# Optimization experiments

Hardware: AMD Instinct MI355X
Metric: run time of the kernel (lower is better)

Reference implementation:

```python
import jax, jax.numpy as jnp
import numpy as np

N_NODES = 50000
N_EDGES = 600000
IN_CH = 128
HID = 128
OUT_CH = 1
N_GRAPHS = 64


def setup_inputs() -> dict:
    key = jax.random.key(0)
    ks = jax.random.split(key, 16)
    inp = {
        "x": jax.random.normal(ks[0], (N_NODES, IN_CH), dtype=jnp.float32),
        "edge_index": jax.random.randint(ks[1], (2, N_EDGES), 0, N_NODES, dtype=jnp.int64),
        "edge_weight": jax.random.uniform(ks[2], (N_EDGES,), dtype=jnp.float32),
        "batch": jnp.sort(jax.random.randint(ks[3], (N_NODES,), 0, N_GRAPHS, dtype=jnp.int64)),
    }
    # SAGEConv params: lin_l (neighbor-aggregate path, has bias) and lin_r (root path)
    dims = [(IN_CH, HID), (HID, HID), (HID, HID), (HID, HID)]
    for i, (din, dout) in enumerate(dims, start=1):
        s = 1.0 / np.sqrt(din)
        inp[f"Wl{i}"] = jax.random.uniform(ks[3 + 2 * i], (din, dout), minval=-s, maxval=s, dtype=jnp.float32)
        inp[f"Wr{i}"] = jax.random.uniform(ks[4 + 2 * i], (din, dout), minval=-s, maxval=s, dtype=jnp.float32)
        inp[f"b{i}"] = jnp.zeros((dout,), dtype=jnp.float32)
    s = 1.0 / np.sqrt(HID)
    inp["Wc"] = jax.random.uniform(ks[14], (HID, OUT_CH), minval=-s, maxval=s, dtype=jnp.float32)
    inp["bc"] = jnp.zeros((OUT_CH,), dtype=jnp.float32)
    return inp


def _sage_conv(x, src, dst, Wl, Wr, b):
    # mean aggregation of source-node features at each destination node
    msg = x[src]  # [E, d] gather
    agg = jax.ops.segment_sum(msg, dst, num_segments=N_NODES)
    cnt = jax.ops.segment_sum(jnp.ones((src.shape[0],), x.dtype), dst, num_segments=N_NODES)
    agg = agg / jnp.maximum(cnt, 1.0)[:, None]
    return agg @ Wl + b + x @ Wr


def reference(x, edge_index, edge_weight, batch,
              Wl1, Wr1, b1, Wl2, Wr2, b2, Wl3, Wr3, b3, Wl4, Wr4, b4, Wc, bc):
    src, dst = edge_index[0], edge_index[1]
    h = jax.nn.relu(_sage_conv(x, src, dst, Wl1, Wr1, b1))
    h = jax.nn.relu(_sage_conv(h, src, dst, Wl2, Wr2, b2))
    h = jax.nn.relu(_sage_conv(h, src, dst, Wl3, Wr3, b3))
    h = jax.nn.relu(_sage_conv(h, src, dst, Wl4, Wr4, b4))
    # global mean pool over graphs
    pooled = jax.ops.segment_sum(h, batch, num_segments=N_GRAPHS)
    gcnt = jax.ops.segment_sum(jnp.ones((N_NODES,), h.dtype), batch, num_segments=N_GRAPHS)
    pooled = pooled / jnp.maximum(gcnt, 1.0)[:, None]  # [G, HID]
    return jax.nn.sigmoid(pooled @ Wc + bc)  # [G, 1]
```

## Files before the change

### kernel.cpp

```cpp
#include <hip/hip_runtime.h>
#include <math.h>

#define NND 50000
#define LNP 50048
#define NED 600000
#define CD  128
#define NG  64
#define NBLK 196
#define GROWS 64

typedef short s8v  __attribute__((ext_vector_type(8)));
typedef float f4v  __attribute__((ext_vector_type(4)));
typedef float f2v  __attribute__((ext_vector_type(2)));
typedef unsigned short u16x4 __attribute__((ext_vector_type(4)));
typedef unsigned short u16x8 __attribute__((ext_vector_type(8)));

static __device__ __forceinline__ unsigned short f2bf(float f) {
  union { float f; unsigned u; } v; v.f = f;
  unsigned r = v.u + 0x7fffu + ((v.u >> 16) & 1u);
  return (unsigned short)(r >> 16);
}
static __device__ __forceinline__ unsigned short f2bf_t(float f) {
  union { float f; unsigned u; } v; v.f = f;
  return (unsigned short)(v.u >> 16);
}
static __device__ __forceinline__ unsigned f2fp8x4(float a, float b, float c, float d) {
  int r = __builtin_amdgcn_cvt_pk_fp8_f32(a, b, 0, false);
  r = __builtin_amdgcn_cvt_pk_fp8_f32(c, d, r, true);
  return (unsigned)r;
}
static __device__ __forceinline__ s8v fp8x8_to_bf16(uint2 v) {
  f2v c0 = __builtin_amdgcn_cvt_pk_f32_fp8(v.x, false);
  f2v c1 = __builtin_amdgcn_cvt_pk_f32_fp8(v.x, true);
  f2v c2 = __builtin_amdgcn_cvt_pk_f32_fp8(v.y, false);
  f2v c3 = __builtin_amdgcn_cvt_pk_f32_fp8(v.y, true);
  union { u16x8 u; s8v s; } o;
  o.u[0] = f2bf_t(c0.x); o.u[1] = f2bf_t(c0.y);
  o.u[2] = f2bf_t(c1.x); o.u[3] = f2bf_t(c1.y);
  o.u[4] = f2bf_t(c2.x); o.u[5] = f2bf_t(c2.y);
  o.u[6] = f2bf_t(c3.x); o.u[7] = f2bf_t(c3.y);
  return o.s;
}
static __device__ __forceinline__ void g2lds8(const unsigned char* g, unsigned char* l) {
  __builtin_amdgcn_global_load_lds(
      (const __attribute__((address_space(1))) unsigned*)g,
      (__attribute__((address_space(3))) unsigned*)l, 16, 0, 0);
}

__global__ __launch_bounds__(256) void bsum_k(const int* __restrict__ cnt,
                                              int* __restrict__ bsum) {
  __shared__ int s[256];
  int i = blockIdx.x * 256 + threadIdx.x;
  s[threadIdx.x] = (i < NND) ? cnt[i] : 0;
  __syncthreads();
  for (int off = 128; off > 0; off >>= 1) {
    if (threadIdx.x < off) s[threadIdx.x] += s[threadIdx.x + off];
    __syncthreads();
  }
  if (threadIdx.x == 0) bsum[blockIdx.x] = s[0];
}

__global__ __launch_bounds__(256) void bscan_k(const int* __restrict__ bsum,
                                               int* __restrict__ boff,
                                               int* __restrict__ offs,
                                               const int* __restrict__ batch,
                                               int* __restrict__ gb) {
  __shared__ int s[256];
  int t = threadIdx.x;
  if (t <= NG) {
    int lo = 0, hi = NND;
    while (lo < hi) {
      int mid = (lo + hi) >> 1;
      if (batch[mid] < t) lo = mid + 1; else hi = mid;
    }
    gb[t] = lo;
  }
  s[t] = (t < NBLK) ? bsum[t] : 0;
  __syncthreads();
  for (int off = 1; off < 256; off <<= 1) {
    int v = (t >= off) ? s[t - off] : 0;
    __syncthreads();
    s[t] += v;
    __syncthreads();
  }
  if (t < NBLK) boff[t] = (t == 0) ? 0 : s[t - 1];
  if (t == NBLK - 1) offs[NND] = s[t];
}

__global__ __launch_bounds__(256) void escan_k(const int* __restrict__ cnt,
                                               const int* __restrict__ boff,
                                               int* __restrict__ offs,
                                               int* __restrict__ cur) {
  __shared__ int s[256];
  int i = blockIdx.x * 256 + threadIdx.x;
  int t = threadIdx.x;
  int v = (i < NND) ? cnt[i] : 0;
  s[t] = v;
  __syncthreads();
  for (int off = 1; off < 256; off <<= 1) {
    int u = (t >= off) ? s[t - off] : 0;
    __syncthreads();
    s[t] += u;
    __syncthreads();
  }
  if (i < NND) {
    int excl = s[t] - v + boff[blockIdx.x];
    offs[i] = excl;
    cur[i]  = excl;
  }
}

__global__ void fill_k(const int* __restrict__ src, const int* __restrict__ dst,
                       int* __restrict__ cur, int* __restrict__ csr) {
  int e = blockIdx.x * blockDim.x + threadIdx.x;
  if (e >= NED) return;
  int d = dst[e];
  int pos = atomicAdd(&cur[d], 1);
  csr[pos] = src[e];
}

struct WPtrs { const float* w[8]; unsigned short* wt[8]; };
__global__ void prep_k(const float* __restrict__ x, unsigned* __restrict__ x8,
                       WPtrs p, const int* __restrict__ dst, int* __restrict__ cnt) {
  int t = blockIdx.x * blockDim.x + threadIdx.x;
  if (t < NND * 32) {
    float4 v = reinterpret_cast<const float4*>(x)[t];
    x8[t] = f2fp8x4(v.x, v.y, v.z, v.w);
  } else {
    int u = t - NND * 32;
    if (u < 8 * CD * CD) {
      int m = u >> 14, r = u & (CD * CD - 1);
      int n = r >> 7, k = r & 127;
      p.wt[m][r] = f2bf(p.w[m][k * CD + n]);
    } else {
      int e = u - 8 * CD * CD;
      if (e < NED) atomicAdd(&cnt[dst[e]], 1);
    }
  }
}

__global__ __launch_bounds__(256, 4) void sage_k(
    const unsigned* __restrict__ xq,
    const int* __restrict__ csr, const int* __restrict__ offs,
    const unsigned short* __restrict__ WlT, const unsigned short* __restrict__ WrT,
    const float* __restrict__ bias, unsigned char* __restrict__ h8,
    const int* __restrict__ batch, float* __restrict__ pooled) {
  __shared__ unsigned short abuf[GROWS * CD];
  __shared__ unsigned char  x8buf[GROWS * CD];
  __shared__ int sB[GROWS];

  const int tid  = threadIdx.x;
  const int wave = tid >> 6;
  const int lane = tid & 63;
  const int quad = lane >> 4;
  const int l16  = lane & 15;
  const size_t rbase = (size_t)blockIdx.x * GROWS;

  {
    const unsigned char* xg = (const unsigned char*)xq;
#pragma unroll
    for (int j = 0; j < 2; ++j) {
      const int s = j * 256 + tid;
      g2lds8(xg + (rbase + (s >> 3)) * CD + (s & 7) * 16, &x8buf[(size_t)s * 16]);
    }
  }

  if (pooled && tid < GROWS) {
    size_t row = rbase + tid;
    sB[tid] = (row < NND) ? batch[row] : -1;
  }

  s8v bL[2][4], bR[2][4];
#pragma unroll
  for (int nt = 0; nt < 2; ++nt) {
    const int n = wave * 32 + nt * 16 + l16;
#pragma unroll
    for (int kk = 0; kk < 4; ++kk) {
      size_t woff = (size_t)n * CD + kk * 32 + quad * 8;
      bL[nt][kk] = *reinterpret_cast<const s8v*>(WlT + woff);
      bR[nt][kk] = *reinterpret_cast<const s8v*>(WrT + woff);
    }
  }
  const float bv0 = bias[wave * 32 + l16];
  const float bv1 = bias[wave * 32 + 16 + l16];

  {
    const int team = tid >> 3;
    const int tl   = tid & 7;
    const unsigned* base = xq + tl * 4;
    for (int i = 0; i < 2; ++i) {
      const int rl = team * 2 + i;
      const size_t row = rbase + rl;
      u16x8 o0 = {}, o1 = {};
      if (row < NND) {
        const int e0 = offs[row], e1 = offs[row + 1];
        f2v a[8] = {};
        int e = e0;
        for (; e + 4 <= e1; e += 4) {
          int s[4];
#pragma unroll
          for (int j = 0; j < 4; ++j) s[j] = csr[e + j];
          uint4 v[4];
#pragma unroll
          for (int j = 0; j < 4; ++j)
            v[j] = *reinterpret_cast<const uint4*>(base + (size_t)s[j] * 32);
#pragma unroll
          for (int j = 0; j < 4; ++j) {
            a[0] += __builtin_amdgcn_cvt_pk_f32_fp8(v[j].x, false);
            a[1] += __builtin_amdgcn_cvt_pk_f32_fp8(v[j].x, true);
            a[2] += __builtin_amdgcn_cvt_pk_f32_fp8(v[j].y, false);
            a[3] += __builtin_amdgcn_cvt_pk_f32_fp8(v[j].y, true);
            a[4] += __builtin_amdgcn_cvt_pk_f32_fp8(v[j].z, false);
            a[5] += __builtin_amdgcn_cvt_pk_f32_fp8(v[j].z, true);
            a[6] += __builtin_amdgcn_cvt_pk_f32_fp8(v[j].w, false);
            a[7] += __builtin_amdgcn_cvt_pk_f32_fp8(v[j].w, true);
          }
        }
        for (; e < e1; ++e) {
          uint4 v = *reinterpret_cast<const uint4*>(base + (size_t)csr[e] * 32);
          a[0] += __builtin_amdgcn_cvt_pk_f32_fp8(v.x, false);
          a[1] += __builtin_amdgcn_cvt_pk_f32_fp8(v.x, true);
          a[2] += __builtin_amdgcn_cvt_pk_f32_fp8(v.y, false);
          a[3] += __builtin_amdgcn_cvt_pk_f32_fp8(v.y, true);
          a[4] += __builtin_amdgcn_cvt_pk_f32_fp8(v.z, false);
          a[5] += __builtin_amdgcn_cvt_pk_f32_fp8(v.z, true);
          a[6] += __builtin_amdgcn_cvt_pk_f32_fp8(v.w, false);
          a[7] += __builtin_amdgcn_cvt_pk_f32_fp8(v.w, true);
        }
        const float invd = 1.0f / fmaxf((float)(e1 - e0), 1.0f);
#pragma unroll
        for (int c = 0; c < 4; ++c) {
          o0[2 * c]     = f2bf(a[c].x * invd);
          o0[2 * c + 1] = f2bf(a[c].y * invd);
          o1[2 * c]     = f2bf(a[4 + c].x * invd);
          o1[2 * c + 1] = f2bf(a[4 + c].y * invd);
        }
      }
      *reinterpret_cast<u16x8*>(abuf + rl * CD + tl * 16)     = o0;
      *reinterpret_cast<u16x8*>(abuf + rl * CD + tl * 16 + 8) = o1;
    }
  }

  __syncthreads();

  const bool fast = pooled && (rbase + GROWS <= NND) && (sB[0] == sB[GROWS - 1]);
  const int c0 = wave * 32 + l16;
  float p0 = 0.f, p1 = 0.f;

#pragma unroll
  for (int rt = 0; rt < GROWS / 16; ++rt) {
    const unsigned short* arow = abuf + (rt * 16 + l16) * CD + quad * 8;
    const unsigned char*  xrow = x8buf + (rt * 16 + l16) * CD + quad * 8;
    f4v acc0 = {}, acc1 = {};
#pragma unroll
    for (int kk = 0; kk < 4; ++kk) {
      s8v aA = *reinterpret_cast<const s8v*>(arow + kk * 32);
      s8v aX = fp8x8_to_bf16(*reinterpret_cast<const uint2*>(xrow + kk * 32));
      acc0 = __builtin_amdgcn_mfma_f32_16x16x32_bf16(aA, bL[0][kk], acc0, 0, 0, 0);
      acc0 = __builtin_amdgcn_mfma_f32_16x16x32_bf16(aX, bR[0][kk], acc0, 0, 0, 0);
      acc1 = __builtin_amdgcn_mfma_f32_16x16x32_bf16(aA, bL[1][kk], acc1, 0, 0, 0);
      acc1 = __builtin_amdgcn_mfma_f32_16x16x32_bf16(aX, bR[1][kk], acc1, 0, 0, 0);
    }
    const size_t row0 = rbase + rt * 16 + quad * 4;
#pragma unroll
    for (int r = 0; r < 4; ++r) {
      const size_t row = row0 + r;
      float v0 = fmaxf(acc0[r] + bv0, 0.0f);
      float v1 = fmaxf(acc1[r] + bv1, 0.0f);
      if (h8) {
        int q0 = __builtin_amdgcn_cvt_pk_fp8_f32(v0, v0, 0, false);
        int q1 = __builtin_amdgcn_cvt_pk_fp8_f32(v1, v1, 0, false);
        h8[row * CD + c0]      = (unsigned char)q0;
        h8[row * CD + c0 + 16] = (unsigned char)q1;
      }
      if (pooled) {
        if (fast) {
          p0 += v0; p1 += v1;
        } else {
          int g = sB[rt * 16 + quad * 4 + r];
          if (g >= 0) {
            atomicAdd(&pooled[g * CD + c0], v0);
            atomicAdd(&pooled[g * CD + c0 + 16], v1);
          }
        }
      }
    }
  }

  if (fast) {
    p0 += __shfl_xor(p0, 16, 64);
    p0 += __shfl_xor(p0, 32, 64);
    p1 += __shfl_xor(p1, 16, 64);
    p1 += __shfl_xor(p1, 32, 64);
    if (quad == 0) {
      const int g = sB[0];
      atomicAdd(&pooled[g * CD + c0], p0);
      atomicAdd(&pooled[g * CD + c0 + 16], p1);
    }
  }
}

__global__ void final_k(const float* __restrict__ pooled, const int* __restrict__ gb,
                        const float* __restrict__ Wc, const float* __restrict__ bc,
                        float* __restrict__ out) {
  int g = blockIdx.x;
  int lane = threadIdx.x;
  float part = pooled[g * CD + lane] * Wc[lane] +
               pooled[g * CD + 64 + lane] * Wc[64 + lane];
#pragma unroll
  for (int off = 32; off > 0; off >>= 1) part += __shfl_down(part, off, 64);
  if (lane == 0) {
    float cnt = (float)(gb[g + 1] - gb[g]);
    float z = part / fmaxf(cnt, 1.0f) + bc[0];
    out[g] = 1.0f / (1.0f + expf(-z));
  }
}

extern "C" void kernel_launch(void* const* d_in, const int* in_sizes, int n_in,
                              void* d_out, int out_size, void* d_ws, size_t ws_size,
                              hipStream_t stream) {
  const float* x   = (const float*)d_in[0];
  const int*   ei  = (const int*)d_in[1];
  const int*   src = ei;
  const int*   dst = ei + NED;
  const int*   batch = (const int*)d_in[3];
  const float* Wc = (const float*)d_in[16];
  const float* bc = (const float*)d_in[17];
  float* out = (float*)d_out;

  char* w = (char*)d_ws;
  auto alloc = [&](size_t bytes) {
    char* p = w; w += (bytes + 255) & ~(size_t)255; return p;
  };
  int* cnti = (int*)alloc(NND * 4);
  float* pooled = (float*)alloc(NG * CD * 4);
  size_t zspan = (size_t)(w - (char*)cnti);
  int* offs = (int*)alloc((NND + 1) * 4);
  int* cur  = (int*)alloc(NND * 4);
  int* csr  = (int*)alloc((size_t)NED * 4);
  int* gb   = (int*)alloc((NG + 1) * 4);
  int* bsum = (int*)alloc(256 * 4);
  int* boff = (int*)alloc(256 * 4);
  unsigned char* x8a = (unsigned char*)alloc((size_t)LNP * CD);
  unsigned char* x8b = (unsigned char*)alloc((size_t)LNP * CD);
  WPtrs wp;
  for (int i = 0; i < 4; ++i) {
    wp.w[2 * i]     = (const float*)d_in[4 + 3 * i];
    wp.w[2 * i + 1] = (const float*)d_in[5 + 3 * i];
  }
  for (int i = 0; i < 8; ++i) wp.wt[i] = (unsigned short*)alloc(CD * CD * 2);
  const float* bs[4] = {(const float*)d_in[6],  (const float*)d_in[9],
                        (const float*)d_in[12], (const float*)d_in[15]};

  hipMemsetAsync(cnti, 0, zspan, stream);

  prep_k<<<(NND * 32 + 8 * CD * CD + NED + 255) / 256, 256, 0, stream>>>(
      x, (unsigned*)x8a, wp, dst, cnti);

  bsum_k<<<NBLK, 256, 0, stream>>>(cnti, bsum);
  bscan_k<<<1, 256, 0, stream>>>(bsum, boff, offs, batch, gb);
  escan_k<<<NBLK, 256, 0, stream>>>(cnti, boff, offs, cur);
  fill_k<<<(NED + 255) / 256, 256, 0, stream>>>(src, dst, cur, csr);

  unsigned char* qcur = x8a;
  unsigned char* qnxt = x8b;
  const int ggrid = LNP / GROWS;
  for (int l = 0; l < 4; ++l) {
    if (l < 3) {
      sage_k<<<ggrid, 256, 0, stream>>>((const unsigned*)qcur, csr, offs,
                                        wp.wt[2 * l], wp.wt[2 * l + 1], bs[l],
                                        qnxt, batch, nullptr);
      unsigned char* q = qcur; qcur = qnxt; qnxt = q;
    } else {
      sage_k<<<ggrid, 256, 0, stream>>>((const unsigned*)qcur, csr, offs,
                                        wp.wt[2 * l], wp.wt[2 * l + 1], bs[l],
                                        nullptr, batch, pooled);
    }
  }

  final_k<<<NG, 64, 0, stream>>>(pooled, gb, Wc, bc, out);
}
```

Measured before the change: 310.2 us.

## Fuse four SAGE layers and final head into one cooperative persistent kernel

Replaces the four per-layer sage_k launches and the final_k launch with a single cooperative kernel that loops over layers with grid-wide syncs between them, using persistent blocks that stride over row tiles. It also adds an XOR swizzle to the LDS layouts of the aggregate and root-feature buffers to reduce bank conflicts, and moves the weight register loads after the gather phase. This removes launch gaps and tail effects between layers, at the cost of grid-barrier overhead, fewer resident blocks than tiles, and extra intermediate buffers.

Measured after the change: 983.3 us. +217.0%, slower.

```diff
diff --git a/kernel.cpp b/kernel.cpp
--- a/kernel.cpp
+++ b/kernel.cpp
@@ -1,5 +1,8 @@
 #include <hip/hip_runtime.h>
+#include <hip/hip_cooperative_groups.h>
 #include <math.h>
+
+namespace cg = cooperative_groups;
 
 #define NND 50000
 #define LNP 50048
@@ -8,11 +11,11 @@
 #define NG  64
 #define NBLK 196
 #define GROWS 64
+#define GGRID (LNP / GROWS)
 
 typedef short s8v  __attribute__((ext_vector_type(8)));
 typedef float f4v  __attribute__((ext_vector_type(4)));
 typedef float f2v  __attribute__((ext_vector_type(2)));
-typedef unsigned short u16x4 __attribute__((ext_vector_type(4)));
 typedef unsigned short u16x8 __attribute__((ext_vector_type(8)));
 
 static __device__ __forceinline__ unsigned short f2bf(float f) {
@@ -139,29 +142,32 @@
   }
 }
 
-__global__ __launch_bounds__(256, 4) void sage_k(
+struct WT8 { const unsigned short* w[8]; };
+struct BP4 { const float* b[4]; };
+
+static __device__ __forceinline__ void sage_tile(
+    int tile,
     const unsigned* __restrict__ xq,
     const int* __restrict__ csr, const int* __restrict__ offs,
     const unsigned short* __restrict__ WlT, const unsigned short* __restrict__ WrT,
     const float* __restrict__ bias, unsigned char* __restrict__ h8,
-    const int* __restrict__ batch, float* __restrict__ pooled) {
-  __shared__ unsigned short abuf[GROWS * CD];
-  __shared__ unsigned char  x8buf[GROWS * CD];
-  __shared__ int sB[GROWS];
-
+    const int* __restrict__ batch, float* __restrict__ pooled,
+    unsigned short* abuf, unsigned char* x8buf, int* sB) {
   const int tid  = threadIdx.x;
   const int wave = tid >> 6;
   const int lane = tid & 63;
   const int quad = lane >> 4;
   const int l16  = lane & 15;
-  const size_t rbase = (size_t)blockIdx.x * GROWS;
+  const size_t rbase = (size_t)tile * GROWS;
 
   {
     const unsigned char* xg = (const unsigned char*)xq;
 #pragma unroll
     for (int j = 0; j < 2; ++j) {
       const int s = j * 256 + tid;
-      g2lds8(xg + (rbase + (s >> 3)) * CD + (s & 7) * 16, &x8buf[(size_t)s * 16]);
+      const int row = s >> 3;
+      const int c = (s & 7) ^ (row & 7);
+      g2lds8(xg + (rbase + row) * CD + c * 16, &x8buf[(size_t)s * 16]);
     }
   }
 
@@ -169,20 +175,6 @@
     size_t row = rbase + tid;
     sB[tid] = (row < NND) ? batch[row] : -1;
   }
-
-  s8v bL[2][4], bR[2][4];
-#pragma unroll
-  for (int nt = 0; nt < 2; ++nt) {
-    const int n = wave * 32 + nt * 16 + l16;
-#pragma unroll
-    for (int kk = 0; kk < 4; ++kk) {
-      size_t woff = (size_t)n * CD + kk * 32 + quad * 8;
-      bL[nt][kk] = *reinterpret_cast<const s8v*>(WlT + woff);
-      bR[nt][kk] = *reinterpret_cast<const s8v*>(WrT + woff);
-    }
-  }
-  const float bv0 = bias[wave * 32 + l16];
-  const float bv1 = bias[wave * 32 + 16 + l16];
 
   {
     const int team = tid >> 3;
@@ -236,10 +228,26 @@
           o1[2 * c + 1] = f2bf(a[4 + c].y * invd);
         }
       }
-      *reinterpret_cast<u16x8*>(abuf + rl * CD + tl * 16)     = o0;
-      *reinterpret_cast<u16x8*>(abuf + rl * CD + tl * 16 + 8) = o1;
-    }
-  }
+      char* ab = (char*)(abuf + rl * CD);
+      const int swr = rl & 7;
+      *reinterpret_cast<u16x8*>(ab + ((((tl << 1))     ^ swr) << 4)) = o0;
+      *reinterpret_cast<u16x8*>(ab + ((((tl << 1) | 1) ^ swr) << 4)) = o1;
+    }
+  }
+
+  s8v bL[2][4], bR[2][4];
+#pragma unroll
+  for (int nt = 0; nt < 2; ++nt) {
+    const int n = wave * 32 + nt * 16 + l16;
+#pragma unroll
+    for (int kk = 0; kk < 4; ++kk) {
+      size_t woff = (size_t)n * CD + kk * 32 + quad * 8;
+      bL[nt][kk] = *reinterpret_cast<const s8v*>(WlT + woff);
+      bR[nt][kk] = *reinterpret_cast<const s8v*>(WrT + woff);
+    }
+  }
+  const float bv0 = bias[wave * 32 + l16];
+  const float bv1 = bias[wave * 32 + 16 + l16];
 
   __syncthreads();
 
@@ -249,13 +257,17 @@
 
 #pragma unroll
   for (int rt = 0; rt < GROWS / 16; ++rt) {
-    const unsigned short* arow = abuf + (rt * 16 + l16) * CD + quad * 8;
-    const unsigned char*  xrow = x8buf + (rt * 16 + l16) * CD + quad * 8;
+    const int row = rt * 16 + l16;
+    const int sw  = row & 7;
+    const char* arow = (const char*)(abuf + row * CD);
+    const char* xrow = (const char*)(x8buf + row * CD);
     f4v acc0 = {}, acc1 = {};
 #pragma unroll
     for (int kk = 0; kk < 4; ++kk) {
-      s8v aA = *reinterpret_cast<const s8v*>(arow + kk * 32);
-      s8v aX = fp8x8_to_bf16(*reinterpret_cast<const uint2*>(xrow + kk * 32));
+      s8v aA = *reinterpret_cast<const s8v*>(arow + (((quad + kk * 4) ^ sw) << 4));
+      uint2 xv = *reinterpret_cast<const uint2*>(
+          xrow + ((((quad >> 1) + kk * 2) ^ sw) << 4) + ((quad & 1) << 3));
+      s8v aX = fp8x8_to_bf16(xv);
       acc0 = __builtin_amdgcn_mfma_f32_16x16x32_bf16(aA, bL[0][kk], acc0, 0, 0, 0);
       acc0 = __builtin_amdgcn_mfma_f32_16x16x32_bf16(aX, bR[0][kk], acc0, 0, 0, 0);
       acc1 = __builtin_amdgcn_mfma_f32_16x16x32_bf16(aA, bL[1][kk], acc1, 0, 0, 0);
@@ -264,14 +276,14 @@
     const size_t row0 = rbase + rt * 16 + quad * 4;
 #pragma unroll
     for (int r = 0; r < 4; ++r) {
-      const size_t row = row0 + r;
+      const size_t orow = row0 + r;
       float v0 = fmaxf(acc0[r] + bv0, 0.0f);
       float v1 = fmaxf(acc1[r] + bv1, 0.0f);
       if (h8) {
         int q0 = __builtin_amdgcn_cvt_pk_fp8_f32(v0, v0, 0, false);
         int q1 = __builtin_amdgcn_cvt_pk_fp8_f32(v1, v1, 0, false);
-        h8[row * CD + c0]      = (unsigned char)q0;
-        h8[row * CD + c0 + 16] = (unsigned char)q1;
+        h8[orow * CD + c0]      = (unsigned char)q0;
+        h8[orow * CD + c0 + 16] = (unsigned char)q1;
       }
       if (pooled) {
         if (fast) {
@@ -298,21 +310,61 @@
       atomicAdd(&pooled[g * CD + c0 + 16], p1);
     }
   }
-}
-
-__global__ void final_k(const float* __restrict__ pooled, const int* __restrict__ gb,
-                        const float* __restrict__ Wc, const float* __restrict__ bc,
-                        float* __restrict__ out) {
-  int g = blockIdx.x;
-  int lane = threadIdx.x;
-  float part = pooled[g * CD + lane] * Wc[lane] +
-               pooled[g * CD + 64 + lane] * Wc[64 + lane];
-#pragma unroll
-  for (int off = 32; off > 0; off >>= 1) part += __shfl_down(part, off, 64);
-  if (lane == 0) {
-    float cnt = (float)(gb[g + 1] - gb[g]);
-    float z = part / fmaxf(cnt, 1.0f) + bc[0];
-    out[g] = 1.0f / (1.0f + expf(-z));
+
+  __syncthreads();
+}
+
+__global__ __launch_bounds__(256, 4) void sage_coop_k(
+    const unsigned* q0, unsigned char* q1, unsigned char* q2, unsigned char* q3,
+    const int* __restrict__ csr, const int* __restrict__ offs,
+    WT8 wt, BP4 bp,
+    const int* __restrict__ batch, float* __restrict__ pooled,
+    const int* __restrict__ gb, const float* __restrict__ Wc,
+    const float* __restrict__ bc, float* __restrict__ out) {
+  cg::grid_group grid = cg::this_grid();
+  __shared__ unsigned short abuf[GROWS * CD];
+  __shared__ unsigned char  x8buf[GROWS * CD];
+  __shared__ int sB[GROWS];
+
+#pragma unroll 1
+  for (int l = 0; l < 4; ++l) {
+    const unsigned* qin = (l == 0) ? q0
+                        : (l == 1) ? (const unsigned*)q1
+                        : (l == 2) ? (const unsigned*)q2
+                                   : (const unsigned*)q3;
+    unsigned char* qout = (l == 0) ? q1 : (l == 1) ? q2 : (l == 2) ? q3 : nullptr;
+    const unsigned short* Wl = (l == 0) ? wt.w[0] : (l == 1) ? wt.w[2]
+                             : (l == 2) ? wt.w[4] : wt.w[6];
+    const unsigned short* Wr = (l == 0) ? wt.w[1] : (l == 1) ? wt.w[3]
+                             : (l == 2) ? wt.w[5] : wt.w[7];
+    const float* bs = (l == 0) ? bp.b[0] : (l == 1) ? bp.b[1]
+                    : (l == 2) ? bp.b[2] : bp.b[3];
+    float* pl = (l == 3) ? pooled : nullptr;
+
+    for (int t = blockIdx.x; t < GGRID; t += gridDim.x)
+      sage_tile(t, qin, csr, offs, Wl, Wr, bs, qout, batch, pl, abuf, x8buf, sB);
+
+    __threadfence();
+    grid.sync();
+    __threadfence();
+  }
+
+  if (blockIdx.x == 0) {
+    const int wv = threadIdx.x >> 6, ln = threadIdx.x & 63;
+    for (int g = wv; g < NG; g += 4) {
+      float a0 = __hip_atomic_load(&pooled[g * CD + ln],
+                                   __ATOMIC_RELAXED, __HIP_MEMORY_SCOPE_AGENT);
+      float a1 = __hip_atomic_load(&pooled[g * CD + 64 + ln],
+                                   __ATOMIC_RELAXED, __HIP_MEMORY_SCOPE_AGENT);
+      float part = a0 * Wc[ln] + a1 * Wc[64 + ln];
+#pragma unroll
+      for (int off = 32; off > 0; off >>= 1) part += __shfl_down(part, off, 64);
+      if (ln == 0) {
+        float cnt = (float)(gb[g + 1] - gb[g]);
+        float z = part / fmaxf(cnt, 1.0f) + bc[0];
+        out[g] = 1.0f / (1.0f + expf(-z));
+      }
+    }
   }
 }
 
@@ -343,6 +395,8 @@
   int* boff = (int*)alloc(256 * 4);
   unsigned char* x8a = (unsigned char*)alloc((size_t)LNP * CD);
   unsigned char* x8b = (unsigned char*)alloc((size_t)LNP * CD);
+  unsigned char* x8c = (unsigned char*)alloc((size_t)LNP * CD);
+  unsigned char* x8d = (unsigned char*)alloc((size_t)LNP * CD);
   WPtrs wp;
   for (int i = 0; i < 4; ++i) {
     wp.w[2 * i]     = (const float*)d_in[4 + 3 * i];
@@ -362,21 +416,29 @@
   escan_k<<<NBLK, 256, 0, stream>>>(cnti, boff, offs, cur);
   fill_k<<<(NED + 255) / 256, 256, 0, stream>>>(src, dst, cur, csr);
 
-  unsigned char* qcur = x8a;
-  unsigned char* qnxt = x8b;
-  const int ggrid = LNP / GROWS;
-  for (int l = 0; l < 4; ++l) {
-    if (l < 3) {
-      sage_k<<<ggrid, 256, 0, stream>>>((const unsigned*)qcur, csr, offs,
-                                        wp.wt[2 * l], wp.wt[2 * l + 1], bs[l],
-                                        qnxt, batch, nullptr);
-      unsigned char* q = qcur; qcur = qnxt; qnxt = q;
-    } else {
-      sage_k<<<ggrid, 256, 0, stream>>>((const unsigned*)qcur, csr, offs,
-                                        wp.wt[2 * l], wp.wt[2 * l + 1], bs[l],
-                                        nullptr, batch, pooled);
-    }
-  }
-
-  final_k<<<NG, 64, 0, stream>>>(pooled, gb, Wc, bc, out);
-}
+  static int coopGrid = 0;
+  if (coopGrid == 0) {
+    int occ = 0;
+    hipOccupancyMaxActiveBlocksPerMultiprocessor(&occ, sage_coop_k, 256, 0);
+    if (occ < 1) occ = 1;
+    long cap = (long)occ * 256;
+    coopGrid = (int)((cap < GGRID) ? cap : GGRID);
+  }
+  WT8 wt8; for (int i = 0; i < 8; ++i) wt8.w[i] = wp.wt[i];
+  BP4 bp4; for (int i = 0; i < 4; ++i) bp4.b[i] = bs[i];
+  const unsigned* a_q0 = (const unsigned*)x8a;
+  unsigned char* a_q1 = x8b;
+  unsigned char* a_q2 = x8c;
+  unsigned char* a_q3 = x8d;
+  const int* a_csr = csr;
+  const int* a_offs = offs;
+  const int* a_batch = batch;
+  float* a_pooled = pooled;
+  const int* a_gb = gb;
+  const float* a_Wc = Wc;
+  const float* a_bc = bc;
+  float* a_out = out;
+  void* args[] = {&a_q0, &a_q1, &a_q2, &a_q3, &a_csr, &a_offs, &wt8, &bp4,
+                  &a_batch, &a_pooled, &a_gb, &a_Wc, &a_bc, &a_out};
+  hipLaunchCooperativeKernel(sage_coop_k, dim3(coopGrid), dim3(256), args, 0, stream);
+}
```

## Halve rows per SAGE block and fuse final readout via last-block pattern

Applied to the files above, without the earlier changes.

Reduces rows per block from 64 to 32, doubling the grid so each thread aggregates one row instead of two. This gives more parallelism and latency hiding for the irregular neighbor gathers. It also removes the separate final_k launch: in the last layer each block increments a done counter, and the last block to finish computes the pooled-mean readout and sigmoid. In exchange it adds fences and an atomic per block, and doubles weight-fragment loads per row across the larger grid.

Measured after the change: 424.5 us. 1.37x slower.

```diff
diff --git a/kernel.cpp b/kernel.cpp
--- a/kernel.cpp
+++ b/kernel.cpp
@@ -7,12 +7,12 @@
 #define CD  128
 #define NG  64
 #define NBLK 196
-#define GROWS 64
+#define GROWS 32
+#define GGRID (LNP / GROWS)
 
 typedef short s8v  __attribute__((ext_vector_type(8)));
 typedef float f4v  __attribute__((ext_vector_type(4)));
 typedef float f2v  __attribute__((ext_vector_type(2)));
-typedef unsigned short u16x4 __attribute__((ext_vector_type(4)));
 typedef unsigned short u16x8 __attribute__((ext_vector_type(8)));
 
 static __device__ __forceinline__ unsigned short f2bf(float f) {
@@ -144,10 +144,14 @@
     const int* __restrict__ csr, const int* __restrict__ offs,
     const unsigned short* __restrict__ WlT, const unsigned short* __restrict__ WrT,
     const float* __restrict__ bias, unsigned char* __restrict__ h8,
-    const int* __restrict__ batch, float* __restrict__ pooled) {
+    const int* __restrict__ batch, float* __restrict__ pooled,
+    int* __restrict__ done, const int* __restrict__ gb,
+    const float* __restrict__ Wc, const float* __restrict__ bc,
+    float* __restrict__ out) {
   __shared__ unsigned short abuf[GROWS * CD];
   __shared__ unsigned char  x8buf[GROWS * CD];
   __shared__ int sB[GROWS];
+  __shared__ int slast;
 
   const int tid  = threadIdx.x;
   const int wave = tid >> 6;
@@ -158,11 +162,8 @@
 
   {
     const unsigned char* xg = (const unsigned char*)xq;
-#pragma unroll
-    for (int j = 0; j < 2; ++j) {
-      const int s = j * 256 + tid;
-      g2lds8(xg + (rbase + (s >> 3)) * CD + (s & 7) * 16, &x8buf[(size_t)s * 16]);
-    }
+    const int s = tid;
+    g2lds8(xg + (rbase + (s >> 3)) * CD + (s & 7) * 16, &x8buf[(size_t)s * 16]);
   }
 
   if (pooled && tid < GROWS) {
@@ -188,57 +189,55 @@
     const int team = tid >> 3;
     const int tl   = tid & 7;
     const unsigned* base = xq + tl * 4;
-    for (int i = 0; i < 2; ++i) {
-      const int rl = team * 2 + i;
-      const size_t row = rbase + rl;
-      u16x8 o0 = {}, o1 = {};
-      if (row < NND) {
-        const int e0 = offs[row], e1 = offs[row + 1];
-        f2v a[8] = {};
-        int e = e0;
-        for (; e + 4 <= e1; e += 4) {
-          int s[4];
-#pragma unroll
-          for (int j = 0; j < 4; ++j) s[j] = csr[e + j];
-          uint4 v[4];
-#pragma unroll
-          for (int j = 0; j < 4; ++j)
-            v[j] = *reinterpret_cast<const uint4*>(base + (size_t)s[j] * 32);
-#pragma unroll
-          for (int j = 0; j < 4; ++j) {
-            a[0] += __builtin_amdgcn_cvt_pk_f32_fp8(v[j].x, false);
-            a[1] += __builtin_amdgcn_cvt_pk_f32_fp8(v[j].x, true);
-            a[2] += __builtin_amdgcn_cvt_pk_f32_fp8(v[j].y, false);
-            a[3] += __builtin_amdgcn_cvt_pk_f32_fp8(v[j].y, true);
-            a[4] += __builtin_amdgcn_cvt_pk_f32_fp8(v[j].z, false);
-            a[5] += __builtin_amdgcn_cvt_pk_f32_fp8(v[j].z, true);
-            a[6] += __builtin_amdgcn_cvt_pk_f32_fp8(v[j].w, false);
-            a[7] += __builtin_amdgcn_cvt_pk_f32_fp8(v[j].w, true);
-          }
+    const int rl = team;
+    const size_t row = rbase + rl;
+    u16x8 o0 = {}, o1 = {};
+    if (row < NND) {
+      const int e0 = offs[row], e1 = offs[row + 1];
+      f2v a[8] = {};
+      int e = e0;
+      for (; e + 4 <= e1; e += 4) {
+        int s[4];
+#pragma unroll
+        for (int j = 0; j < 4; ++j) s[j] = csr[e + j];
+        uint4 v[4];
+#pragma unroll
+        for (int j = 0; j < 4; ++j)
+          v[j] = *reinterpret_cast<const uint4*>(base + (size_t)s[j] * 32);
+#pragma unroll
+        for (int j = 0; j < 4; ++j) {
+          a[0] += __builtin_amdgcn_cvt_pk_f32_fp8(v[j].x, false);
+          a[1] += __builtin_amdgcn_cvt_pk_f32_fp8(v[j].x, true);
+          a[2] += __builtin_amdgcn_cvt_pk_f32_fp8(v[j].y, false);
+          a[3] += __builtin_amdgcn_cvt_pk_f32_fp8(v[j].y, true);
+          a[4] += __builtin_amdgcn_cvt_pk_f32_fp8(v[j].z, false);
+          a[5] += __builtin_amdgcn_cvt_pk_f32_fp8(v[j].z, true);
+          a[6] += __builtin_amdgcn_cvt_pk_f32_fp8(v[j].w, false);
+          a[7] += __builtin_amdgcn_cvt_pk_f32_fp8(v[j].w, true);
         }
-        for (; e < e1; ++e) {
-          uint4 v = *reinterpret_cast<const uint4*>(base + (size_t)csr[e] * 32);
-          a[0] += __builtin_amdgcn_cvt_pk_f32_fp8(v.x, false);
-          a[1] += __builtin_amdgcn_cvt_pk_f32_fp8(v.x, true);
-          a[2] += __builtin_amdgcn_cvt_pk_f32_fp8(v.y, false);
-          a[3] += __builtin_amdgcn_cvt_pk_f32_fp8(v.y, true);
-          a[4] += __builtin_amdgcn_cvt_pk_f32_fp8(v.z, false);
-          a[5] += __builtin_amdgcn_cvt_pk_f32_fp8(v.z, true);
-          a[6] += __builtin_amdgcn_cvt_pk_f32_fp8(v.w, false);
-          a[7] += __builtin_amdgcn_cvt_pk_f32_fp8(v.w, true);
-        }
-        const float invd = 1.0f / fmaxf((float)(e1 - e0), 1.0f);
-#pragma unroll
-        for (int c = 0; c < 4; ++c) {
-          o0[2 * c]     = f2bf(a[c].x * invd);
-          o0[2 * c + 1] = f2bf(a[c].y * invd);
-          o1[2 * c]     = f2bf(a[4 + c].x * invd);
-          o1[2 * c + 1] = f2bf(a[4 + c].y * invd);
-        }
-      }
-      *reinterpret_cast<u16x8*>(abuf + rl * CD + tl * 16)     = o0;
-      *reinterpret_cast<u16x8*>(abuf + rl * CD + tl * 16 + 8) = o1;
-    }
+      }
+      for (; e < e1; ++e) {
+        uint4 v = *reinterpret_cast<const uint4*>(base + (size_t)csr[e] * 32);
+        a[0] += __builtin_amdgcn_cvt_pk_f32_fp8(v.x, false);
+        a[1] += __builtin_amdgcn_cvt_pk_f32_fp8(v.x, true);
+        a[2] += __builtin_amdgcn_cvt_pk_f32_fp8(v.y, false);
+        a[3] += __builtin_amdgcn_cvt_pk_f32_fp8(v.y, true);
+        a[4] += __builtin_amdgcn_cvt_pk_f32_fp8(v.z, false);
+        a[5] += __builtin_amdgcn_cvt_pk_f32_fp8(v.z, true);
+        a[6] += __builtin_amdgcn_cvt_pk_f32_fp8(v.w, false);
+        a[7] += __builtin_amdgcn_cvt_pk_f32_fp8(v.w, true);
+      }
+      const float invd = 1.0f / fmaxf((float)(e1 - e0), 1.0f);
+#pragma unroll
+      for (int c = 0; c < 4; ++c) {
+        o0[2 * c]     = f2bf(a[c].x * invd);
+        o0[2 * c + 1] = f2bf(a[c].y * invd);
+        o1[2 * c]     = f2bf(a[4 + c].x * invd);
+        o1[2 * c + 1] = f2bf(a[4 + c].y * invd);
+      }
+    }
+    *reinterpret_cast<u16x8*>(abuf + rl * CD + tl * 16)     = o0;
+    *reinterpret_cast<u16x8*>(abuf + rl * CD + tl * 16 + 8) = o1;
   }
 
   __syncthreads();
@@ -287,6 +286,8 @@
     }
   }
 
+  if (!pooled) return;
+
   if (fast) {
     p0 += __shfl_xor(p0, 16, 64);
     p0 += __shfl_xor(p0, 32, 64);
@@ -298,21 +299,30 @@
       atomicAdd(&pooled[g * CD + c0 + 16], p1);
     }
   }
-}
-
-__global__ void final_k(const float* __restrict__ pooled, const int* __restrict__ gb,
-                        const float* __restrict__ Wc, const float* __restrict__ bc,
-                        float* __restrict__ out) {
-  int g = blockIdx.x;
-  int lane = threadIdx.x;
-  float part = pooled[g * CD + lane] * Wc[lane] +
-               pooled[g * CD + 64 + lane] * Wc[64 + lane];
-#pragma unroll
-  for (int off = 32; off > 0; off >>= 1) part += __shfl_down(part, off, 64);
-  if (lane == 0) {
-    float cnt = (float)(gb[g + 1] - gb[g]);
-    float z = part / fmaxf(cnt, 1.0f) + bc[0];
-    out[g] = 1.0f / (1.0f + expf(-z));
+
+  __threadfence();
+  if (tid == 0) {
+    int prev = __hip_atomic_fetch_add(done, 1, __ATOMIC_ACQ_REL,
+                                      __HIP_MEMORY_SCOPE_AGENT);
+    slast = (prev == GGRID - 1) ? 1 : 0;
+  }
+  __syncthreads();
+  if (slast) {
+    const int wv = tid >> 6, ln = tid & 63;
+    for (int g = wv; g < NG; g += 4) {
+      float a0 = __hip_atomic_load(&pooled[g * CD + ln],
+                                   __ATOMIC_RELAXED, __HIP_MEMORY_SCOPE_AGENT);
+      float a1 = __hip_atomic_load(&pooled[g * CD + 64 + ln],
+                                   __ATOMIC_RELAXED, __HIP_MEMORY_SCOPE_AGENT);
+      float part = a0 * Wc[ln] + a1 * Wc[64 + ln];
+#pragma unroll
+      for (int off = 32; off > 0; off >>= 1) part += __shfl_down(part, off, 64);
+      if (ln == 0) {
+        float cnt = (float)(gb[g + 1] - gb[g]);
+        float z = part / fmaxf(cnt, 1.0f) + bc[0];
+        out[g] = 1.0f / (1.0f + expf(-z));
+      }
+    }
   }
 }
 
@@ -334,6 +344,7 @@
   };
   int* cnti = (int*)alloc(NND * 4);
   float* pooled = (float*)alloc(NG * CD * 4);
+  int* done = (int*)alloc(4);
   size_t zspan = (size_t)(w - (char*)cnti);
   int* offs = (int*)alloc((NND + 1) * 4);
   int* cur  = (int*)alloc(NND * 4);
@@ -364,19 +375,18 @@
 
   unsigned char* qcur = x8a;
   unsigned char* qnxt = x8b;
-  const int ggrid = LNP / GROWS;
   for (int l = 0; l < 4; ++l) {
     if (l < 3) {
-      sage_k<<<ggrid, 256, 0, stream>>>((const unsigned*)qcur, csr, offs,
+      sage_k<<<GGRID, 256, 0, stream>>>((const unsigned*)qcur, csr, offs,
                                         wp.wt[2 * l], wp.wt[2 * l + 1], bs[l],
-                                        qnxt, batch, nullptr);
+                                        qnxt, batch, nullptr,
+                                        done, gb, Wc, bc, out);
       unsigned char* q = qcur; qcur = qnxt; qnxt = q;
     } else {
-      sage_k<<<ggrid, 256, 0, stream>>>((const unsigned*)qcur, csr, offs,
+      sage_k<<<GGRID, 256, 0, stream>>>((const unsigned*)qcur, csr, offs,
                                         wp.wt[2 * l], wp.wt[2 * l + 1], bs[l],
-                                        nullptr, batch, pooled);
-    }
-  }
-
-  final_k<<<NG, 64, 0, stream>>>(pooled, gb, Wc, bc, out);
-}
+                                        nullptr, batch, pooled,
+                                        done, gb, Wc, bc, out);
+    }
+  }
+}
```
